# Performance work log

Measured on AMD Instinct MI355X. Metric: run time of the kernel, lower is better.

## Reference

```python
import jax, jax.numpy as jnp
import numpy as np


def setup_inputs() -> dict:
    key = jax.random.key(0)
    k1, k2 = jax.random.split(key)
    B, C, H, W = 16, 256, 64, 64
    K, D = 1024, 256
    z = jax.random.normal(k1, (B, C, H, W), dtype=jnp.float32)
    embedding = jax.random.normal(k2, (K, D), dtype=jnp.float32)
    return {"z": z, "embedding": embedding}


def reference(z, embedding):
    # _preprocess: shift channel dim (axis 1) to last, flatten -> [N, D]
    B, C, H, W = z.shape
    encoded_permuted = jnp.transpose(z, (0, 2, 3, 1))  # [B, H, W, C]
    permuted_shape = encoded_permuted.shape
    encoded_flat = encoded_permuted.reshape(-1, C)  # [N, D]

    x_sq = jnp.sum(encoded_flat * encoded_flat, axis=1, keepdims=True)  # [N, 1]
    e_sq = jnp.sum(embedding * embedding, axis=1)  # [K]
    cross = encoded_flat @ embedding.T  # [N, K]
    distances = x_sq - 2.0 * cross + e_sq[None, :]
    codebook_indices = jnp.argmin(distances, axis=1)  # [N]
    quantized_lookup = embedding[codebook_indices]  # [N, D]

    # straight-through estimator
    quantized_flat = encoded_flat + jax.lax.stop_gradient(quantized_lookup - encoded_flat)

    # _postprocess: reshape and shift last dim back to axis 1
    quantized = jnp.transpose(quantized_flat.reshape(permuted_shape), (0, 3, 1, 2))
    return (encoded_flat, quantized_flat, codebook_indices, quantized)
```

## Files before the change

kernel.cpp:

```cpp
#include <hip/hip_runtime.h>
#include <hip/hip_bf16.h>

typedef _Float16 h8 __attribute__((ext_vector_type(8)));
typedef float f4 __attribute__((ext_vector_type(4)));

#define N_TOK 65536
#define DIM 256
#define KCODES 1024
#define HWSZ 4096

__device__ __forceinline__ void gll16(const void* g, void* l) {
    __builtin_amdgcn_global_load_lds((const __attribute__((address_space(1))) void*)g,
                                     (__attribute__((address_space(3))) void*)l, 16, 0, 0);
}


__global__ void k_prep_frag(const float* __restrict__ emb, _Float16* __restrict__ BhF,
                            _Float16* __restrict__ BlF) {
    int gi = blockIdx.x * 256 + threadIdx.x;
    int kb = gi >> 9;
    int s = (gi >> 6) & 7;
    int dq = (gi >> 4) & 3;
    int r = gi & 15;
    int code = kb * 16 + r;
    int d0 = s * 32 + dq * 8;
    const float* src = emb + (size_t)code * DIM + d0;
    float4 x0 = *(const float4*)(src);
    float4 x1 = *(const float4*)(src + 4);
    float xs[8] = {x0.x, x0.y, x0.z, x0.w, x1.x, x1.y, x1.z, x1.w};
    h8 hi, lo;
#pragma unroll
    for (int j = 0; j < 8; ++j) {
        _Float16 h = (_Float16)xs[j];
        hi[j] = h;
        lo[j] = (_Float16)(xs[j] - (float)h);
    }
    *(h8*)(BhF + (size_t)gi * 8) = hi;
    *(h8*)(BlF + (size_t)gi * 8) = lo;
}

__global__ void k_esq(const float* __restrict__ emb, float* __restrict__ e_sq) {
    int t = threadIdx.x;
    int code = blockIdx.x * 4 + (t >> 6);
    int l = t & 63;
    float4 v = *(const float4*)(emb + (size_t)code * DIM + l * 4);
    float s = v.x * v.x + v.y * v.y + v.z * v.z + v.w * v.w;
#pragma unroll
    for (int off = 32; off >= 1; off >>= 1) s += __shfl_xor(s, off);
    if (l == 0) e_sq[code] = s;
}

__global__ void k_transpose(const float* __restrict__ z, float* __restrict__ enc,
                            _Float16* __restrict__ AhF, _Float16* __restrict__ AlF) {
    __shared__ float T[64][65];
    int blk = blockIdx.x;
    int b = blk >> 8;
    int rem = blk & 255;
    int c0 = (rem >> 6) * 64;
    int hw0 = (rem & 63) * 64;
    int t = threadIdx.x;
    const float* zp = z + (size_t)b * DIM * HWSZ;
    {
        int hw4 = (t & 15) * 4, cl = t >> 4;
#pragma unroll
        for (int i = 0; i < 4; ++i) {
            int c = cl + i * 16;
            float4 v = *(const float4*)(zp + (size_t)(c0 + c) * HWSZ + hw0 + hw4);
            T[c][hw4 + 0] = v.x; T[c][hw4 + 1] = v.y;
            T[c][hw4 + 2] = v.z; T[c][hw4 + 3] = v.w;
        }
    }
    __syncthreads();
    {
        int c4 = (t & 15) * 4, hwl = t >> 4;
#pragma unroll
        for (int i = 0; i < 4; ++i) {
            int hw = hwl + i * 16;
            float4 v;
            v.x = T[c4 + 0][hw]; v.y = T[c4 + 1][hw];
            v.z = T[c4 + 2][hw]; v.w = T[c4 + 3][hw];
            *(float4*)(enc + (size_t)(b * HWSZ + hw0 + hw) * DIM + c0 + c4) = v;
        }
    }
    {
        int base_nb = b * 256 + (hw0 >> 4);
#pragma unroll
        for (int i = 0; i < 2; ++i) {
            int gidx = i * 256 + t;
            int nbi = gidx >> 7;
            int si = (gidx >> 6) & 1;
            int dq = (gidx >> 4) & 3;
            int r = gidx & 15;
            int hwl = nbi * 16 + r;
            int cl = si * 32 + dq * 8;
            h8 hi, lo;
#pragma unroll
            for (int j = 0; j < 8; ++j) {
                float x = T[cl + j][hwl];
                _Float16 h = (_Float16)x;
                hi[j] = h;
                lo[j] = (_Float16)(x - (float)h);
            }
            size_t G = (((size_t)(base_nb + nbi) * 8) + (c0 >> 5) + si) * 64 + dq * 16 + r;
            *(h8*)(AhF + G * 8) = hi;
            *(h8*)(AlF + G * 8) = lo;
        }
    }
}

#define WAITV(n) asm volatile("s_waitcnt vmcnt(" #n ")" ::: "memory")
#define BARRIER __builtin_amdgcn_s_barrier()
#define PRIO1 __builtin_amdgcn_s_setprio(1)
#define PRIO0 __builtin_amdgcn_s_setprio(0)

extern __shared__ char SB[];

__global__ __launch_bounds__(1024)
void k_gemm_argmin(const _Float16* __restrict__ AhF, const _Float16* __restrict__ AlF,
                   const _Float16* __restrict__ BhF, const _Float16* __restrict__ BlF,
                   const float* __restrict__ e_sq,
                   float* __restrict__ pV1, int* __restrict__ pI1) {
    int gid = blockIdx.x;
    int colTile = gid >> 8;
    int rowTile = gid & 255;
    int r0 = rowTile * 256, c0 = colTile * 256;
    int t = threadIdx.x;
    int w = t >> 6, l = t & 63;
    int wm = w >> 2, wn = w & 3;
    int l16 = l & 15, lhi = l >> 4;

    const char* gAh = (const char*)AhF + (((size_t)(rowTile * 16 + w)) << 13) + (l << 4);
    const char* gAl = (const char*)AlF + (((size_t)(rowTile * 16 + w)) << 13) + (l << 4);
    const char* gBh = (const char*)BhF + (((size_t)(colTile * 16 + w)) << 13) + (l << 4);
    const char* gBl = (const char*)BlF + (((size_t)(colTile * 16 + w)) << 13) + (l << 4);

#define ISSUE_P(p) do { \
    const int s_ = (p) >> 1; \
    char* bp_ = SB + ((p) & 3) * 32768; \
    const char* a_ = ((p) & 1) ? gAl : gAh; \
    const char* b_ = ((p) & 1) ? gBl : gBh; \
    gll16(a_ + (s_ << 10), bp_ + (w << 10)); \
    gll16(b_ + (s_ << 10), bp_ + 16384 + (w << 10)); \
} while (0)

#define MFMA16(A_, B_) { _Pragma("unroll") for (int mf = 0; mf < 4; ++mf) \
    _Pragma("unroll") for (int nf = 0; nf < 4; ++nf) \
        acc[mf][nf] = __builtin_amdgcn_mfma_f32_16x16x32_f16(A_[mf], B_[nf], acc[mf][nf], 0, 0, 0); }

#define PHASE(q, W, DO_ISSUE) { \
    WAITV(W); \
    BARRIER; \
    if (DO_ISSUE) ISSUE_P((q) + 3); \
    const char* bp_ = SB + ((q) & 3) * 32768; \
    if (((q) & 1) == 0) { \
        _Pragma("unroll") for (int mf = 0; mf < 4; ++mf) \
            ah[mf] = *(const h8*)(bp_ + ((wm * 4 + mf) << 10) + (l << 4)); \
        _Pragma("unroll") for (int nf = 0; nf < 4; ++nf) \
            bh[nf] = *(const h8*)(bp_ + 16384 + ((wn * 4 + nf) << 10) + (l << 4)); \
        PRIO1; MFMA16(ah, bh); PRIO0; \
    } else { \
        h8 xl[4]; \
        _Pragma("unroll") for (int nf = 0; nf < 4; ++nf) \
            xl[nf] = *(const h8*)(bp_ + 16384 + ((wn * 4 + nf) << 10) + (l << 4)); \
        PRIO1; MFMA16(ah, xl); PRIO0; \
        _Pragma("unroll") for (int mf = 0; mf < 4; ++mf) \
            xl[mf] = *(const h8*)(bp_ + ((wm * 4 + mf) << 10) + (l << 4)); \
        PRIO1; MFMA16(xl, bh); PRIO0; \
    } }

    f4 acc[4][4];
#pragma unroll
    for (int i = 0; i < 4; ++i)
#pragma unroll
        for (int j = 0; j < 4; ++j) acc[i][j] = (f4)0.0f;

    h8 ah[4], bh[4];

    ISSUE_P(0); ISSUE_P(1); ISSUE_P(2);

    PHASE(0, 4, 1)   PHASE(1, 4, 1)   PHASE(2, 4, 1)   PHASE(3, 4, 1)
    PHASE(4, 4, 1)   PHASE(5, 4, 1)   PHASE(6, 4, 1)   PHASE(7, 4, 1)
    PHASE(8, 4, 1)   PHASE(9, 4, 1)   PHASE(10, 4, 1)  PHASE(11, 4, 1)
    PHASE(12, 4, 1)  PHASE(13, 4, 0)  PHASE(14, 2, 0)  PHASE(15, 0, 0)

    float* smV = (float*)SB;
    int* smI = (int*)(SB + 4096);

    float esq[4];
#pragma unroll
    for (int nf = 0; nf < 4; ++nf) esq[nf] = e_sq[c0 + wn * 64 + nf * 16 + l16];

#pragma unroll
    for (int mf = 0; mf < 4; ++mf) {
#pragma unroll
        for (int rg = 0; rg < 4; ++rg) {
            float bestV = 3.4e38f;
            int bestI = 0;
#pragma unroll
            for (int nf = 0; nf < 4; ++nf) {
                float v = esq[nf] - 2.0f * acc[mf][nf][rg];
                int ci = c0 + wn * 64 + nf * 16 + l16;
                if (v < bestV || (v == bestV && ci < bestI)) { bestV = v; bestI = ci; }
            }
#pragma unroll
            for (int off = 1; off < 16; off <<= 1) {
                float vv = __shfl_xor(bestV, off);
                int ii = __shfl_xor(bestI, off);
                if (vv < bestV || (vv == bestV && ii < bestI)) { bestV = vv; bestI = ii; }
            }
            if (l16 == 0) {
                int rloc = wm * 64 + mf * 16 + lhi * 4 + rg;
                smV[wn * 256 + rloc] = bestV;
                smI[wn * 256 + rloc] = bestI;
            }
        }
    }
    __syncthreads();
    if (t < 256) {
        float bestV = smV[t];
        int bestI = smI[t];
#pragma unroll
        for (int wn2 = 1; wn2 < 4; ++wn2) {
            float v = smV[wn2 * 256 + t];
            int i2 = smI[wn2 * 256 + t];
            if (v < bestV || (v == bestV && i2 < bestI)) { bestV = v; bestI = i2; }
        }
        pV1[colTile * N_TOK + r0 + t] = bestV;
        pI1[colTile * N_TOK + r0 + t] = bestI;
    }
}

__global__ void k_final_out1(const float* __restrict__ pV1, const int* __restrict__ pI1,
                             const float* __restrict__ emb,
                             float* __restrict__ out2, int* __restrict__ idxI,
                             float* __restrict__ out1) {
    __shared__ int sidx[256];
    int t = threadIdx.x;
    int n0 = blockIdx.x * 256;
    int n = n0 + t;
    float v1 = pV1[n];
    int i1 = pI1[n];
#pragma unroll
    for (int ct = 1; ct < 4; ++ct) {
        float a1 = pV1[ct * N_TOK + n];
        int ai = pI1[ct * N_TOK + n];
        if (a1 < v1 || (a1 == v1 && ai < i1)) { v1 = a1; i1 = ai; }
    }
    out2[n] = (float)i1;
    idxI[n] = i1;
    sidx[t] = i1;
    __syncthreads();
    int rr = t >> 2, q = t & 3;
#pragma unroll
    for (int i = 0; i < 4; ++i) {
        int r = i * 64 + rr;
        int idx = sidx[r];
        const float* src = emb + (size_t)idx * DIM + q * 64;
        float* dst = out1 + (size_t)(n0 + r) * DIM + q * 64;
#pragma unroll
        for (int j = 0; j < 16; ++j)
            *(float4*)(dst + j * 4) = *(const float4*)(src + j * 4);
    }
}

__global__ void k_out3(const float* __restrict__ emb, const int* __restrict__ idxI,
                       float* __restrict__ out3) {
    __shared__ float E[32][257];
    int blk = blockIdx.x;
    int b = blk >> 7, hwt = blk & 127;
    int hw0 = hwt * 32;
    int n0 = b * HWSZ + hw0;
    int t = threadIdx.x;
    {
        int r = t >> 3, oct = t & 7;
        int idx = idxI[n0 + r];
        const float* src = emb + (size_t)idx * DIM + oct * 32;
#pragma unroll
        for (int i = 0; i < 8; ++i) {
            float4 v = *(const float4*)(src + i * 4);
            E[r][oct * 32 + i * 4 + 0] = v.x;
            E[r][oct * 32 + i * 4 + 1] = v.y;
            E[r][oct * 32 + i * 4 + 2] = v.z;
            E[r][oct * 32 + i * 4 + 3] = v.w;
        }
    }
    __syncthreads();
    {
        int w = t >> 6, l = t & 63;
        int ch = l >> 5, hw = l & 31;
        float* dst = out3 + (size_t)b * DIM * HWSZ + hw0 + hw;
#pragma unroll
        for (int it = 0; it < 32; ++it) {
            int c = w * 64 + it * 2 + ch;
            dst[(size_t)c * HWSZ] = E[hw][c];
        }
    }
}

extern "C" void kernel_launch(void* const* d_in, const int* in_sizes, int n_in,
                              void* d_out, int out_size, void* d_ws, size_t ws_size,
                              hipStream_t stream) {
    const float* z = (const float*)d_in[0];
    const float* emb = (const float*)d_in[1];
    float* out = (float*)d_out;
    float* out0 = out;
    float* out1 = out + 16777216;
    float* out2 = out + 33554432;
    float* out3 = out + 33619968;

    _Float16* AhF = (_Float16*)out1;
    _Float16* AlF = (_Float16*)(out1 + 8388608);

    char* ws = (char*)d_ws;
    _Float16* BhF = (_Float16*)(ws);
    _Float16* BlF = (_Float16*)(ws + 524288);
    float* e_sq = (float*)(ws + 1048576);
    float* pV1 = (float*)(ws + 1052672);
    int* pI1 = (int*)(ws + 2101248);
    int* idxI = (int*)(ws + 3149824);

    static bool attr_set = false;
    if (!attr_set) {
        hipFuncSetAttribute((const void*)k_gemm_argmin,
                            hipFuncAttributeMaxDynamicSharedMemorySize, 131072);
        attr_set = true;
    }

    k_prep_frag<<<128, 256, 0, stream>>>(emb, BhF, BlF);
    k_esq<<<256, 256, 0, stream>>>(emb, e_sq);
    k_transpose<<<4096, 256, 0, stream>>>(z, out0, AhF, AlF);
    k_gemm_argmin<<<1024, 1024, 131072, stream>>>(AhF, AlF, BhF, BlF, e_sq, pV1, pI1);
    k_final_out1<<<256, 256, 0, stream>>>(pV1, pI1, emb, out2, idxI, out1);
    k_out3<<<2048, 256, 0, stream>>>(emb, idxI, out3);
}
```

Measured before the change: 222.4 us.

## Loop over all codebook tiles per block and fuse final argmin and gather

Each GEMM block now walks all four 256-code column tiles in one persistent loop, prefetching the next tile's B fragments across tile boundaries. It keeps a running argmin in shared memory, then writes the indices and gathers the embedding rows into out1 directly, so the partial-result buffers and the k_final_out1 launch go away. The grid drops from 1024 to 256 blocks of 1024 threads, so on this GPU there is roughly one block per CU and less parallel slack. LDS use grows to about 140 KB, and the A staging buffers move into out3.

```diff
diff --git a/kernel.cpp b/kernel.cpp
--- a/kernel.cpp
+++ b/kernel.cpp
@@ -118,12 +118,11 @@
 __global__ __launch_bounds__(1024)
 void k_gemm_argmin(const _Float16* __restrict__ AhF, const _Float16* __restrict__ AlF,
                    const _Float16* __restrict__ BhF, const _Float16* __restrict__ BlF,
-                   const float* __restrict__ e_sq,
-                   float* __restrict__ pV1, int* __restrict__ pI1) {
-    int gid = blockIdx.x;
-    int colTile = gid >> 8;
-    int rowTile = gid & 255;
-    int r0 = rowTile * 256, c0 = colTile * 256;
+                   const float* __restrict__ e_sq, const float* __restrict__ emb,
+                   float* __restrict__ out1, float* __restrict__ out2,
+                   int* __restrict__ idxI) {
+    int rowTile = blockIdx.x;
+    int r0 = rowTile * 256;
     int t = threadIdx.x;
     int w = t >> 6, l = t & 63;
     int wm = w >> 2, wn = w & 3;
@@ -131,26 +130,33 @@
 
     const char* gAh = (const char*)AhF + (((size_t)(rowTile * 16 + w)) << 13) + (l << 4);
     const char* gAl = (const char*)AlF + (((size_t)(rowTile * 16 + w)) << 13) + (l << 4);
-    const char* gBh = (const char*)BhF + (((size_t)(colTile * 16 + w)) << 13) + (l << 4);
-    const char* gBl = (const char*)BlF + (((size_t)(colTile * 16 + w)) << 13) + (l << 4);
-
-#define ISSUE_P(p) do { \
-    const int s_ = (p) >> 1; \
-    char* bp_ = SB + ((p) & 3) * 32768; \
-    const char* a_ = ((p) & 1) ? gAl : gAh; \
-    const char* b_ = ((p) & 1) ? gBl : gBh; \
+    const char* gBh = (const char*)BhF + (((size_t)w) << 13) + (l << 4);
+    const char* gBl = (const char*)BlF + (((size_t)w) << 13) + (l << 4);
+
+    float* smV = (float*)(SB + 131072);
+    int*   smI = (int*)(SB + 135168);
+    int*  sidx = (int*)(SB + 139264);
+
+#define ISSUE_Q(ctoff, q2) do { \
+    const int s_ = (q2) >> 1; \
+    char* bp_ = SB + ((q2) & 3) * 32768; \
+    const char* a_ = ((q2) & 1) ? gAl : gAh; \
+    const char* b_ = ((q2) & 1) ? gBl : gBh; \
     gll16(a_ + (s_ << 10), bp_ + (w << 10)); \
-    gll16(b_ + (s_ << 10), bp_ + 16384 + (w << 10)); \
+    gll16(b_ + (ctoff) + (s_ << 10), bp_ + 16384 + (w << 10)); \
 } while (0)
 
 #define MFMA16(A_, B_) { _Pragma("unroll") for (int mf = 0; mf < 4; ++mf) \
     _Pragma("unroll") for (int nf = 0; nf < 4; ++nf) \
         acc[mf][nf] = __builtin_amdgcn_mfma_f32_16x16x32_f16(A_[mf], B_[nf], acc[mf][nf], 0, 0, 0); }
 
-#define PHASE(q, W, DO_ISSUE) { \
-    WAITV(W); \
+#define PHASE(q) { \
+    if ((q) == 14) { if (lastct) { WAITV(2); } else { WAITV(4); } } \
+    else if ((q) == 15) { if (lastct) { WAITV(0); } else { WAITV(4); } } \
+    else { WAITV(4); } \
     BARRIER; \
-    if (DO_ISSUE) ISSUE_P((q) + 3); \
+    if ((q) <= 12) { ISSUE_Q(ctoff, (q) + 3); } \
+    else if (!lastct) { ISSUE_Q(ctoffN, (q) - 13); } \
     const char* bp_ = SB + ((q) & 3) * 32768; \
     if (((q) & 1) == 0) { \
         _Pragma("unroll") for (int mf = 0; mf < 4; ++mf) \
@@ -175,88 +181,77 @@
         for (int j = 0; j < 4; ++j) acc[i][j] = (f4)0.0f;
 
     h8 ah[4], bh[4];
-
-    ISSUE_P(0); ISSUE_P(1); ISSUE_P(2);
-
-    PHASE(0, 4, 1)   PHASE(1, 4, 1)   PHASE(2, 4, 1)   PHASE(3, 4, 1)
-    PHASE(4, 4, 1)   PHASE(5, 4, 1)   PHASE(6, 4, 1)   PHASE(7, 4, 1)
-    PHASE(8, 4, 1)   PHASE(9, 4, 1)   PHASE(10, 4, 1)  PHASE(11, 4, 1)
-    PHASE(12, 4, 1)  PHASE(13, 4, 0)  PHASE(14, 2, 0)  PHASE(15, 0, 0)
-
-    float* smV = (float*)SB;
-    int* smI = (int*)(SB + 4096);
-
-    float esq[4];
-#pragma unroll
-    for (int nf = 0; nf < 4; ++nf) esq[nf] = e_sq[c0 + wn * 64 + nf * 16 + l16];
-
-#pragma unroll
-    for (int mf = 0; mf < 4; ++mf) {
-#pragma unroll
-        for (int rg = 0; rg < 4; ++rg) {
-            float bestV = 3.4e38f;
-            int bestI = 0;
-#pragma unroll
-            for (int nf = 0; nf < 4; ++nf) {
-                float v = esq[nf] - 2.0f * acc[mf][nf][rg];
-                int ci = c0 + wn * 64 + nf * 16 + l16;
-                if (v < bestV || (v == bestV && ci < bestI)) { bestV = v; bestI = ci; }
+    float rV = 3.4e38f;
+    int rI = 0;
+
+    ISSUE_Q(0, 0); ISSUE_Q(0, 1); ISSUE_Q(0, 2);
+
+    for (int ct = 0; ct < 4; ++ct) {
+        const bool lastct = (ct == 3);
+        const int ctoff = ct << 17, ctoffN = (ct + 1) << 17;
+
+        PHASE(0)  PHASE(1)  PHASE(2)  PHASE(3)
+        PHASE(4)  PHASE(5)  PHASE(6)  PHASE(7)
+        PHASE(8)  PHASE(9)  PHASE(10) PHASE(11)
+        PHASE(12) PHASE(13) PHASE(14) PHASE(15)
+
+        float esqv[4];
+#pragma unroll
+        for (int nf = 0; nf < 4; ++nf)
+            esqv[nf] = e_sq[ct * 256 + wn * 64 + nf * 16 + l16];
+#pragma unroll
+        for (int mf = 0; mf < 4; ++mf) {
+#pragma unroll
+            for (int rg = 0; rg < 4; ++rg) {
+                float bv = 3.4e38f;
+                int bi = 0;
+#pragma unroll
+                for (int nf = 0; nf < 4; ++nf) {
+                    float v = fmaf(-2.0f, acc[mf][nf][rg], esqv[nf]);
+                    int ci = ct * 256 + wn * 64 + nf * 16 + l16;
+                    if (v < bv) { bv = v; bi = ci; }
+                }
+#pragma unroll
+                for (int off = 1; off < 16; off <<= 1) {
+                    float vv = __shfl_xor(bv, off);
+                    int ii = __shfl_xor(bi, off);
+                    if (vv < bv || (vv == bv && ii < bi)) { bv = vv; bi = ii; }
+                }
+                if (l16 == 0) {
+                    int rloc = wm * 64 + mf * 16 + lhi * 4 + rg;
+                    smV[wn * 256 + rloc] = bv;
+                    smI[wn * 256 + rloc] = bi;
+                }
             }
-#pragma unroll
-            for (int off = 1; off < 16; off <<= 1) {
-                float vv = __shfl_xor(bestV, off);
-                int ii = __shfl_xor(bestI, off);
-                if (vv < bestV || (vv == bestV && ii < bestI)) { bestV = vv; bestI = ii; }
+        }
+#pragma unroll
+        for (int mf = 0; mf < 4; ++mf)
+#pragma unroll
+            for (int nf = 0; nf < 4; ++nf) acc[mf][nf] = (f4)0.0f;
+        __syncthreads();
+        if (t < 256) {
+#pragma unroll
+            for (int wn2 = 0; wn2 < 4; ++wn2) {
+                float vv = smV[wn2 * 256 + t];
+                int ii = smI[wn2 * 256 + t];
+                if (vv < rV || (vv == rV && ii < rI)) { rV = vv; rI = ii; }
             }
-            if (l16 == 0) {
-                int rloc = wm * 64 + mf * 16 + lhi * 4 + rg;
-                smV[wn * 256 + rloc] = bestV;
-                smI[wn * 256 + rloc] = bestI;
-            }
-        }
+        }
+        __syncthreads();
+    }
+
+    if (t < 256) {
+        int n = r0 + t;
+        out2[n] = (float)rI;
+        idxI[n] = rI;
+        sidx[t] = rI;
     }
     __syncthreads();
-    if (t < 256) {
-        float bestV = smV[t];
-        int bestI = smI[t];
-#pragma unroll
-        for (int wn2 = 1; wn2 < 4; ++wn2) {
-            float v = smV[wn2 * 256 + t];
-            int i2 = smI[wn2 * 256 + t];
-            if (v < bestV || (v == bestV && i2 < bestI)) { bestV = v; bestI = i2; }
-        }
-        pV1[colTile * N_TOK + r0 + t] = bestV;
-        pI1[colTile * N_TOK + r0 + t] = bestI;
-    }
-}
-
-__global__ void k_final_out1(const float* __restrict__ pV1, const int* __restrict__ pI1,
-                             const float* __restrict__ emb,
-                             float* __restrict__ out2, int* __restrict__ idxI,
-                             float* __restrict__ out1) {
-    __shared__ int sidx[256];
-    int t = threadIdx.x;
-    int n0 = blockIdx.x * 256;
-    int n = n0 + t;
-    float v1 = pV1[n];
-    int i1 = pI1[n];
-#pragma unroll
-    for (int ct = 1; ct < 4; ++ct) {
-        float a1 = pV1[ct * N_TOK + n];
-        int ai = pI1[ct * N_TOK + n];
-        if (a1 < v1 || (a1 == v1 && ai < i1)) { v1 = a1; i1 = ai; }
-    }
-    out2[n] = (float)i1;
-    idxI[n] = i1;
-    sidx[t] = i1;
-    __syncthreads();
-    int rr = t >> 2, q = t & 3;
-#pragma unroll
-    for (int i = 0; i < 4; ++i) {
-        int r = i * 64 + rr;
-        int idx = sidx[r];
+    {
+        int row = t >> 2, q = t & 3;
+        int idx = sidx[row];
         const float* src = emb + (size_t)idx * DIM + q * 64;
-        float* dst = out1 + (size_t)(n0 + r) * DIM + q * 64;
+        float* dst = out1 + (size_t)(r0 + row) * DIM + q * 64;
 #pragma unroll
         for (int j = 0; j < 16; ++j)
             *(float4*)(dst + j * 4) = *(const float4*)(src + j * 4);
@@ -308,28 +303,22 @@
     float* out2 = out + 33554432;
     float* out3 = out + 33619968;
 
-    _Float16* AhF = (_Float16*)out1;
-    _Float16* AlF = (_Float16*)(out1 + 8388608);
+    _Float16* AhF = (_Float16*)out3;
+    _Float16* AlF = (_Float16*)(out3 + 8388608);
 
     char* ws = (char*)d_ws;
     _Float16* BhF = (_Float16*)(ws);
     _Float16* BlF = (_Float16*)(ws + 524288);
     float* e_sq = (float*)(ws + 1048576);
-    float* pV1 = (float*)(ws + 1052672);
-    int* pI1 = (int*)(ws + 2101248);
-    int* idxI = (int*)(ws + 3149824);
-
-    static bool attr_set = false;
-    if (!attr_set) {
-        hipFuncSetAttribute((const void*)k_gemm_argmin,
-                            hipFuncAttributeMaxDynamicSharedMemorySize, 131072);
-        attr_set = true;
-    }
+    int* idxI = (int*)(ws + 1052672);
+
+    hipFuncSetAttribute((const void*)k_gemm_argmin,
+                        hipFuncAttributeMaxDynamicSharedMemorySize, 140288);
 
     k_prep_frag<<<128, 256, 0, stream>>>(emb, BhF, BlF);
     k_esq<<<256, 256, 0, stream>>>(emb, e_sq);
     k_transpose<<<4096, 256, 0, stream>>>(z, out0, AhF, AlF);
-    k_gemm_argmin<<<1024, 1024, 131072, stream>>>(AhF, AlF, BhF, BlF, e_sq, pV1, pI1);
-    k_final_out1<<<256, 256, 0, stream>>>(pV1, pI1, emb, out2, idxI, out1);
+    k_gemm_argmin<<<256, 1024, 140288, stream>>>(AhF, AlF, BhF, BlF, e_sq, emb,
+                                                 out1, out2, idxI);
     k_out3<<<2048, 256, 0, stream>>>(emb, idxI, out3);
 }
```

Result: slower. 286.0 us (+28.6%).
